# Performance work log

Hardware: AMD Instinct MI355X
Metric: run time of the kernel (lower is better)

## Reference

```python
import jax, jax.numpy as jnp
from jax import lax
import numpy as np


def setup_inputs() -> dict:
    key = jax.random.key(0)
    k1, k2 = jax.random.split(key)
    x = jax.random.normal(k1, (16, 512, 512, 3), dtype=jnp.float32)
    # raw filter; module draws N(mean=10, scale=1) then normalizes to sum 1
    filt = jax.random.normal(k2, (9, 9, 1, 1), dtype=jnp.float32)
    return {"x": x, "filt": filt}


def _conv_same(a, f):
    # NHWC input, HWIO filter, SAME padding, stride 1
    return lax.conv_general_dilated(
        a, f, window_strides=(1, 1), padding="SAME",
        dimension_numbers=("NHWC", "HWIO", "NHWC"))


def reference(x, filt):
    # Keras: random_normal_variable(mean=10, scale=1) -> shift raw N(0,1) by 10
    f = filt + 10.0
    f = f / jnp.sum(f)                      # normalize BEFORE channel repeat
    f = jnp.tile(f, (1, 1, 3, 1))           # (9,9,3,1): sums over 3 input channels
    local_mean = _conv_same(x, f)           # (B,H,W,1), broadcasts over channels
    v = x - local_mean                      # (B,H,W,3)
    sigma = jnp.sqrt(_conv_same(v * v, f))  # (B,H,W,1)
    mean = jnp.mean(sigma, axis=(1, 2), keepdims=True)  # (B,1,1,1)
    return v / jnp.maximum(mean, sigma)
```

## Files before the change

### kernel.cpp

```cpp
#include <hip/hip_runtime.h>

#define BATCH 16
#define HH 512
#define WW 512
#define NPIX (BATCH * HH * WW)

#define RAD 4
#define OT 32
#define MT (OT + 2*RAD)
#define ST (MT + 2*RAD)

__global__ __launch_bounds__(256) void lcn_fused_kernel(
        const float* __restrict__ x, const float* __restrict__ filt,
        float* __restrict__ m, float* __restrict__ sig,
        float* __restrict__ partial) {
    __shared__ float s48[ST][ST];
    __shared__ float q48[ST][ST];
    __shared__ float t40[MT][MT];
    __shared__ float fs[81];
    __shared__ float fsum_sh;
    __shared__ float wsum[4];

    const int tid = threadIdx.x;
    const int b = blockIdx.z;
    const int h0 = blockIdx.y * OT;
    const int w0 = blockIdx.x * OT;
    const float* xb = x + (size_t)b * HH * WW * 3;

    if (tid < 64) {
        float v = filt[tid] + 10.0f;
        if (tid < 17) v += filt[tid + 64] + 10.0f;
#pragma unroll
        for (int o = 32; o > 0; o >>= 1) v += __shfl_down(v, o);
        if (tid == 0) fsum_sh = v;
    }

    for (int i = tid; i < ST * ST; i += 256) {
        int r = i / ST, c = i - r * ST;
        int gh = h0 - 2 * RAD + r, gw = w0 - 2 * RAD + c;
        float sv = 0.0f, qv = 0.0f;
        if (gh >= 0 && gh < HH && gw >= 0 && gw < WW) {
            const float* xp = xb + ((size_t)gh * WW + gw) * 3;
            float a0 = xp[0], a1 = xp[1], a2 = xp[2];
            sv = a0 + a1 + a2;
            qv = a0 * a0 + a1 * a1 + a2 * a2;
        }
        s48[r][c] = sv;
        q48[r][c] = qv;
    }
    __syncthreads();

    if (tid < 81) fs[tid] = (filt[tid] + 10.0f) / fsum_sh;
    __syncthreads();

    {
        const int c2 = tid % MT;
        const int g = tid / MT;
        if (g < 6) {
            const int rbeg = g * 7;
            const int rcnt = (rbeg + 7 <= MT) ? 7 : (MT - rbeg);
            float acc[7] = {0.f, 0.f, 0.f, 0.f, 0.f, 0.f, 0.f};
            for (int tr = 0; tr < rcnt + 8; tr++) {
                float v[9];
#pragma unroll
                for (int j = 0; j < 9; j++) v[j] = s48[rbeg + tr][c2 + j];
#pragma unroll
                for (int o = 0; o < 7; o++) {
                    const int dh = tr - o;
                    if (o < rcnt && dh >= 0 && dh < 9) {
                        float a = 0.0f;
#pragma unroll
                        for (int j = 0; j < 9; j++) a += v[j] * fs[dh * 9 + j];
                        acc[o] += a;
                    }
                }
            }
            for (int o = 0; o < rcnt; o++) {
                const int rr = rbeg + o;
                const int gh = h0 - RAD + rr, gw = w0 - RAD + c2;
                const float mv = acc[o];
                const float sc = s48[rr + RAD][c2 + RAD];
                const float qc = q48[rr + RAD][c2 + RAD];
                const bool inimg = (gh >= 0 && gh < HH && gw >= 0 && gw < WW);
                t40[rr][c2] = inimg ? (qc - 2.0f * mv * sc + 3.0f * mv * mv)
                                    : 0.0f;
                if (rr >= RAD && rr < RAD + OT && c2 >= RAD && c2 < RAD + OT) {
                    m[((size_t)b * HH + gh) * WW + gw] = mv;
                }
            }
        }
    }
    __syncthreads();

    float psum = 0.0f;
    {
        const int c3 = tid % OT;
        const int g3 = tid / OT;
        const int rbeg = g3 * 4;
        float acc[4] = {0.f, 0.f, 0.f, 0.f};
#pragma unroll
        for (int tr = 0; tr < 12; tr++) {
            float v[9];
#pragma unroll
            for (int j = 0; j < 9; j++) v[j] = t40[rbeg + tr][c3 + j];
#pragma unroll
            for (int o = 0; o < 4; o++) {
                const int dh = tr - o;
                if (dh >= 0 && dh < 9) {
                    float a = 0.0f;
#pragma unroll
                    for (int j = 0; j < 9; j++) a += v[j] * fs[dh * 9 + j];
                    acc[o] += a;
                }
            }
        }
#pragma unroll
        for (int o = 0; o < 4; o++) {
            const float sg = sqrtf(fmaxf(acc[o], 0.0f));
            const int h = h0 + rbeg + o, w = w0 + c3;
            sig[((size_t)b * HH + h) * WW + w] = sg;
            psum += sg;
        }
    }

#pragma unroll
    for (int o = 32; o > 0; o >>= 1) psum += __shfl_down(psum, o);
    if ((tid & 63) == 0) wsum[tid >> 6] = psum;
    __syncthreads();
    if (tid == 0)
        partial[b * 256 + blockIdx.y * 16 + blockIdx.x] =
            wsum[0] + wsum[1] + wsum[2] + wsum[3];
}

__global__ __launch_bounds__(256) void reduce_bsum_kernel(
        const float* __restrict__ partial, float* __restrict__ bsum) {
    __shared__ float wsum[4];
    const int b = blockIdx.x, tid = threadIdx.x;
    float v = partial[b * 256 + tid];
#pragma unroll
    for (int o = 32; o > 0; o >>= 1) v += __shfl_down(v, o);
    if ((tid & 63) == 0) wsum[tid >> 6] = v;
    __syncthreads();
    if (tid == 0) bsum[b] = wsum[0] + wsum[1] + wsum[2] + wsum[3];
}

__global__ __launch_bounds__(256) void final_kernel(
        const float* __restrict__ x, const float* __restrict__ m,
        const float* __restrict__ sig, const float* __restrict__ bsum,
        float* __restrict__ out) {
    const int i = blockIdx.x * 256 + threadIdx.x;
    const int b = i >> 16;
    const float mean = bsum[b] * (1.0f / (HH * WW));

    float4 mv = ((const float4*)m)[i];
    float4 sv = ((const float4*)sig)[i];
    const float4* xp = (const float4*)x + (size_t)i * 3;
    float4 a = xp[0], bb = xp[1], cc = xp[2];

    float d0 = fmaxf(mean, sv.x);
    float d1 = fmaxf(mean, sv.y);
    float d2 = fmaxf(mean, sv.z);
    float d3 = fmaxf(mean, sv.w);

    float4 o0, o1, o2;
    o0.x = (a.x - mv.x) / d0;
    o0.y = (a.y - mv.x) / d0;
    o0.z = (a.z - mv.x) / d0;
    o0.w = (a.w - mv.y) / d1;
    o1.x = (bb.x - mv.y) / d1;
    o1.y = (bb.y - mv.y) / d1;
    o1.z = (bb.z - mv.z) / d2;
    o1.w = (bb.w - mv.z) / d2;
    o2.x = (cc.x - mv.z) / d2;
    o2.y = (cc.y - mv.w) / d3;
    o2.z = (cc.z - mv.w) / d3;
    o2.w = (cc.w - mv.w) / d3;

    float4* op = (float4*)out + (size_t)i * 3;
    op[0] = o0;
    op[1] = o1;
    op[2] = o2;
}

extern "C" void kernel_launch(void* const* d_in, const int* in_sizes, int n_in,
                              void* d_out, int out_size, void* d_ws, size_t ws_size,
                              hipStream_t stream) {
    const float* x = (const float*)d_in[0];
    const float* filt = (const float*)d_in[1];
    float* out = (float*)d_out;

    char* ws = (char*)d_ws;
    float* bsum = (float*)(ws + 512);
    float* partial = (float*)(ws + 1024);
    float* m = (float*)(ws + 32768);
    float* sig = m + NPIX;

    dim3 cgrid(WW / OT, HH / OT, BATCH);
    lcn_fused_kernel<<<cgrid, 256, 0, stream>>>(x, filt, m, sig, partial);
    reduce_bsum_kernel<<<BATCH, 256, 0, stream>>>(partial, bsum);
    final_kernel<<<NPIX / 4 / 256, 256, 0, stream>>>(x, m, sig, bsum, out);
}
```

Baseline: 177.4 us.

## Register-block convolutions four columns per thread, precompute filter, use reciprocal

Filter normalization moves to a separate tiny kernel that writes to workspace, so the main kernel reads filter weights from global/constant memory instead of computing them per block. Both convolution passes are reorganized so each thread computes four adjacent output columns from float4 shared-memory loads, with fully unrolled 9x9 loops. This raises ILP and cuts LDS traffic, and the m/sig writes become vectorized. The halo load loop is unrolled, and the final kernel replaces divisions with hardware reciprocal multiplies, which slightly changes precision.

```diff
diff --git a/kernel.cpp b/kernel.cpp
--- a/kernel.cpp
+++ b/kernel.cpp
@@ -10,15 +10,28 @@
 #define MT (OT + 2*RAD)
 #define ST (MT + 2*RAD)
 
+__global__ void norm_filter_kernel(const float* __restrict__ filt,
+                                   float* __restrict__ f) {
+    __shared__ float sh[128];
+    int tid = threadIdx.x;
+    float v = (tid < 81) ? (filt[tid] + 10.0f) : 0.0f;
+    sh[tid] = v;
+    __syncthreads();
+    for (int o = 64; o > 0; o >>= 1) {
+        if (tid < o) sh[tid] += sh[tid + o];
+        __syncthreads();
+    }
+    float sum = sh[0];
+    if (tid < 81) f[tid] = v / sum;
+}
+
 __global__ __launch_bounds__(256) void lcn_fused_kernel(
-        const float* __restrict__ x, const float* __restrict__ filt,
+        const float* __restrict__ x, const float* __restrict__ f,
         float* __restrict__ m, float* __restrict__ sig,
         float* __restrict__ partial) {
     __shared__ float s48[ST][ST];
     __shared__ float q48[ST][ST];
     __shared__ float t40[MT][MT];
-    __shared__ float fs[81];
-    __shared__ float fsum_sh;
     __shared__ float wsum[4];
 
     const int tid = threadIdx.x;
@@ -27,17 +40,11 @@
     const int w0 = blockIdx.x * OT;
     const float* xb = x + (size_t)b * HH * WW * 3;
 
-    if (tid < 64) {
-        float v = filt[tid] + 10.0f;
-        if (tid < 17) v += filt[tid + 64] + 10.0f;
-#pragma unroll
-        for (int o = 32; o > 0; o >>= 1) v += __shfl_down(v, o);
-        if (tid == 0) fsum_sh = v;
-    }
-
-    for (int i = tid; i < ST * ST; i += 256) {
-        int r = i / ST, c = i - r * ST;
-        int gh = h0 - 2 * RAD + r, gw = w0 - 2 * RAD + c;
+#pragma unroll
+    for (int k = 0; k < 9; k++) {
+        const int i = tid + k * 256;
+        const int r = i / ST, c = i - r * ST;
+        const int gh = h0 - 2 * RAD + r, gw = w0 - 2 * RAD + c;
         float sv = 0.0f, qv = 0.0f;
         if (gh >= 0 && gh < HH && gw >= 0 && gw < WW) {
             const float* xp = xb + ((size_t)gh * WW + gw) * 3;
@@ -50,77 +57,84 @@
     }
     __syncthreads();
 
-    if (tid < 81) fs[tid] = (filt[tid] + 10.0f) / fsum_sh;
-    __syncthreads();
-
-    {
-        const int c2 = tid % MT;
-        const int g = tid / MT;
-        if (g < 6) {
-            const int rbeg = g * 7;
-            const int rcnt = (rbeg + 7 <= MT) ? 7 : (MT - rbeg);
-            float acc[7] = {0.f, 0.f, 0.f, 0.f, 0.f, 0.f, 0.f};
-            for (int tr = 0; tr < rcnt + 8; tr++) {
-                float v[9];
-#pragma unroll
-                for (int j = 0; j < 9; j++) v[j] = s48[rbeg + tr][c2 + j];
-#pragma unroll
-                for (int o = 0; o < 7; o++) {
-                    const int dh = tr - o;
-                    if (o < rcnt && dh >= 0 && dh < 9) {
-                        float a = 0.0f;
-#pragma unroll
-                        for (int j = 0; j < 9; j++) a += v[j] * fs[dh * 9 + j];
-                        acc[o] += a;
-                    }
-                }
+    for (int item = tid; item < MT * (MT / 4); item += 256) {
+        const int cg = item % (MT / 4);
+        const int row = item / (MT / 4);
+        const int c0 = 4 * cg;
+
+        float acc0 = 0.f, acc1 = 0.f, acc2 = 0.f, acc3 = 0.f;
+#pragma unroll
+        for (int dh = 0; dh < 9; dh++) {
+            const float4 va = *(const float4*)&s48[row + dh][c0];
+            const float4 vb = *(const float4*)&s48[row + dh][c0 + 4];
+            const float4 vc = *(const float4*)&s48[row + dh][c0 + 8];
+            const float v[12] = {va.x, va.y, va.z, va.w,
+                                 vb.x, vb.y, vb.z, vb.w,
+                                 vc.x, vc.y, vc.z, vc.w};
+#pragma unroll
+            for (int j = 0; j < 9; j++) {
+                const float fv = f[dh * 9 + j];
+                acc0 += v[j] * fv;
+                acc1 += v[j + 1] * fv;
+                acc2 += v[j + 2] * fv;
+                acc3 += v[j + 3] * fv;
             }
-            for (int o = 0; o < rcnt; o++) {
-                const int rr = rbeg + o;
-                const int gh = h0 - RAD + rr, gw = w0 - RAD + c2;
-                const float mv = acc[o];
-                const float sc = s48[rr + RAD][c2 + RAD];
-                const float qc = q48[rr + RAD][c2 + RAD];
-                const bool inimg = (gh >= 0 && gh < HH && gw >= 0 && gw < WW);
-                t40[rr][c2] = inimg ? (qc - 2.0f * mv * sc + 3.0f * mv * mv)
-                                    : 0.0f;
-                if (rr >= RAD && rr < RAD + OT && c2 >= RAD && c2 < RAD + OT) {
-                    m[((size_t)b * HH + gh) * WW + gw] = mv;
-                }
-            }
+        }
+
+        const float4 sc = *(const float4*)&s48[row + 4][c0 + 4];
+        const float4 qc = *(const float4*)&q48[row + 4][c0 + 4];
+        const int gh = h0 - RAD + row;
+        const bool ghin = (gh >= 0 && gh < HH);
+        const int gw0 = w0 - RAD + c0;
+        float4 tv;
+        tv.x = (ghin && gw0 + 0 >= 0 && gw0 + 0 < WW)
+                   ? qc.x - 2.0f * acc0 * sc.x + 3.0f * acc0 * acc0 : 0.0f;
+        tv.y = (ghin && gw0 + 1 >= 0 && gw0 + 1 < WW)
+                   ? qc.y - 2.0f * acc1 * sc.y + 3.0f * acc1 * acc1 : 0.0f;
+        tv.z = (ghin && gw0 + 2 >= 0 && gw0 + 2 < WW)
+                   ? qc.z - 2.0f * acc2 * sc.z + 3.0f * acc2 * acc2 : 0.0f;
+        tv.w = (ghin && gw0 + 3 >= 0 && gw0 + 3 < WW)
+                   ? qc.w - 2.0f * acc3 * sc.w + 3.0f * acc3 * acc3 : 0.0f;
+        *(float4*)&t40[row][c0] = tv;
+
+        if (row >= RAD && row < RAD + OT && cg >= 1 && cg <= 8) {
+            float4 mv4 = {acc0, acc1, acc2, acc3};
+            *(float4*)&m[((size_t)b * HH + gh) * WW + (w0 + 4 * (cg - 1))] = mv4;
         }
     }
     __syncthreads();
 
     float psum = 0.0f;
     {
-        const int c3 = tid % OT;
-        const int g3 = tid / OT;
-        const int rbeg = g3 * 4;
-        float acc[4] = {0.f, 0.f, 0.f, 0.f};
-#pragma unroll
-        for (int tr = 0; tr < 12; tr++) {
-            float v[9];
-#pragma unroll
-            for (int j = 0; j < 9; j++) v[j] = t40[rbeg + tr][c3 + j];
-#pragma unroll
-            for (int o = 0; o < 4; o++) {
-                const int dh = tr - o;
-                if (dh >= 0 && dh < 9) {
-                    float a = 0.0f;
-#pragma unroll
-                    for (int j = 0; j < 9; j++) a += v[j] * fs[dh * 9 + j];
-                    acc[o] += a;
-                }
+        const int cg = tid % (OT / 4);
+        const int row = tid / (OT / 4);
+        const int c0 = 4 * cg;
+
+        float acc0 = 0.f, acc1 = 0.f, acc2 = 0.f, acc3 = 0.f;
+#pragma unroll
+        for (int dh = 0; dh < 9; dh++) {
+            const float4 va = *(const float4*)&t40[row + dh][c0];
+            const float4 vb = *(const float4*)&t40[row + dh][c0 + 4];
+            const float4 vc = *(const float4*)&t40[row + dh][c0 + 8];
+            const float v[12] = {va.x, va.y, va.z, va.w,
+                                 vb.x, vb.y, vb.z, vb.w,
+                                 vc.x, vc.y, vc.z, vc.w};
+#pragma unroll
+            for (int j = 0; j < 9; j++) {
+                const float fv = f[dh * 9 + j];
+                acc0 += v[j] * fv;
+                acc1 += v[j + 1] * fv;
+                acc2 += v[j + 2] * fv;
+                acc3 += v[j + 3] * fv;
             }
         }
-#pragma unroll
-        for (int o = 0; o < 4; o++) {
-            const float sg = sqrtf(fmaxf(acc[o], 0.0f));
-            const int h = h0 + rbeg + o, w = w0 + c3;
-            sig[((size_t)b * HH + h) * WW + w] = sg;
-            psum += sg;
-        }
+        float4 sg;
+        sg.x = sqrtf(fmaxf(acc0, 0.0f));
+        sg.y = sqrtf(fmaxf(acc1, 0.0f));
+        sg.z = sqrtf(fmaxf(acc2, 0.0f));
+        sg.w = sqrtf(fmaxf(acc3, 0.0f));
+        *(float4*)&sig[((size_t)b * HH + (h0 + row)) * WW + (w0 + c0)] = sg;
+        psum = sg.x + sg.y + sg.z + sg.w;
     }
 
 #pragma unroll
@@ -157,24 +171,24 @@
     const float4* xp = (const float4*)x + (size_t)i * 3;
     float4 a = xp[0], bb = xp[1], cc = xp[2];
 
-    float d0 = fmaxf(mean, sv.x);
-    float d1 = fmaxf(mean, sv.y);
-    float d2 = fmaxf(mean, sv.z);
-    float d3 = fmaxf(mean, sv.w);
+    float r0 = __builtin_amdgcn_rcpf(fmaxf(mean, sv.x));
+    float r1 = __builtin_amdgcn_rcpf(fmaxf(mean, sv.y));
+    float r2 = __builtin_amdgcn_rcpf(fmaxf(mean, sv.z));
+    float r3 = __builtin_amdgcn_rcpf(fmaxf(mean, sv.w));
 
     float4 o0, o1, o2;
-    o0.x = (a.x - mv.x) / d0;
-    o0.y = (a.y - mv.x) / d0;
-    o0.z = (a.z - mv.x) / d0;
-    o0.w = (a.w - mv.y) / d1;
-    o1.x = (bb.x - mv.y) / d1;
-    o1.y = (bb.y - mv.y) / d1;
-    o1.z = (bb.z - mv.z) / d2;
-    o1.w = (bb.w - mv.z) / d2;
-    o2.x = (cc.x - mv.z) / d2;
-    o2.y = (cc.y - mv.w) / d3;
-    o2.z = (cc.z - mv.w) / d3;
-    o2.w = (cc.w - mv.w) / d3;
+    o0.x = (a.x - mv.x) * r0;
+    o0.y = (a.y - mv.x) * r0;
+    o0.z = (a.z - mv.x) * r0;
+    o0.w = (a.w - mv.y) * r1;
+    o1.x = (bb.x - mv.y) * r1;
+    o1.y = (bb.y - mv.y) * r1;
+    o1.z = (bb.z - mv.z) * r2;
+    o1.w = (bb.w - mv.z) * r2;
+    o2.x = (cc.x - mv.z) * r2;
+    o2.y = (cc.y - mv.w) * r3;
+    o2.z = (cc.z - mv.w) * r3;
+    o2.w = (cc.w - mv.w) * r3;
 
     float4* op = (float4*)out + (size_t)i * 3;
     op[0] = o0;
@@ -190,13 +204,16 @@
     float* out = (float*)d_out;
 
     char* ws = (char*)d_ws;
+    float* f = (float*)ws;
     float* bsum = (float*)(ws + 512);
     float* partial = (float*)(ws + 1024);
     float* m = (float*)(ws + 32768);
     float* sig = m + NPIX;
 
+    norm_filter_kernel<<<1, 128, 0, stream>>>(filt, f);
+
     dim3 cgrid(WW / OT, HH / OT, BATCH);
-    lcn_fused_kernel<<<cgrid, 256, 0, stream>>>(x, filt, m, sig, partial);
+    lcn_fused_kernel<<<cgrid, 256, 0, stream>>>(x, f, m, sig, partial);
     reduce_bsum_kernel<<<BATCH, 256, 0, stream>>>(partial, bsum);
     final_kernel<<<NPIX / 4 / 256, 256, 0, stream>>>(x, m, sig, bsum, out);
 }
```

Result: no change. 180.1 us (+1.5%).
